# Optimization experiments

Measured on AMD Instinct MI355X. Metric: run time of the kernel, lower is better.

Reference implementation:

```python
import jax, jax.numpy as jnp
import numpy as np

NEG_SLOPE = 0.01  # nn.LeakyReLU default

def _leaky(x):
    return jnp.where(x >= 0, x, NEG_SLOPE * x)

def setup_inputs() -> dict:
    key = jax.random.key(0)
    ks = jax.random.split(key, 8)
    in_ch = 64
    B, H, W = 8, 256, 256
    x = jax.random.normal(ks[0], (B, 2 * in_ch, H, W), dtype=jnp.float32)
    dims = [(64, 128), (32, 64), (16, 32), (8, 16), (4, 8), (2, 4), (1, 2)]
    inp = {"x": x}
    for i, (o, c) in enumerate(dims):
        # kaiming_normal_ fan_out, relu: std = sqrt(2 / fan_out), fan_out = o*1*1
        std = np.sqrt(2.0 / o).astype(np.float32)
        inp[f"w{i+1}"] = jax.random.normal(ks[i + 1], (o, c), dtype=jnp.float32) * std
    return inp

def reference(x, w1, w2, w3, w4, w5, w6, w7):
    # Each 1x1 conv (bias-free) is a per-pixel matmul over channels.
    h = x
    for w in (w1, w2, w3, w4, w5, w6):
        h = _leaky(jnp.einsum('bchw,oc->bohw', h, w))
    out = jnp.einsum('bchw,oc->bohw', h, w7)  # final conv, no activation
    return out
```

## Files before the change

### kernel.cpp

```cpp
#include <hip/hip_runtime.h>


#define NEG_SLOPE 0.01f
constexpr int HW = 65536;

typedef __attribute__((ext_vector_type(8))) short bf16x8;
typedef __attribute__((ext_vector_type(4))) float f32x4;
typedef __attribute__((ext_vector_type(2))) float f32x2;

__device__ __forceinline__ float leaky(float v) { return fmaxf(v, v * NEG_SLOPE); }

__device__ __forceinline__ unsigned pk2(float a, float b) {
    __bf16 ba = (__bf16)a, bb = (__bf16)b;
    unsigned short ua = __builtin_bit_cast(unsigned short, ba);
    unsigned short ub = __builtin_bit_cast(unsigned short, bb);
    return (unsigned)ua | ((unsigned)ub << 16);
}

__device__ __forceinline__ bf16x8 loadA(const float* __restrict__ wsrc, int C, int m, int k) {
    f32x4 lo = *(const f32x4*)(wsrc + m * C + k);
    f32x4 hi = *(const f32x4*)(wsrc + m * C + k + 4);
    union { bf16x8 v; unsigned u[4]; } r;
    r.u[0] = pk2(lo[0], lo[1]); r.u[1] = pk2(lo[2], lo[3]);
    r.u[2] = pk2(hi[0], hi[1]); r.u[3] = pk2(hi[2], hi[3]);
    return r.v;
}

__device__ __forceinline__ void async_cp16(const float* g, float* l) {
    __builtin_amdgcn_global_load_lds((const __attribute__((address_space(1))) unsigned*)g,
                                     (__attribute__((address_space(3))) unsigned*)l,
                                     16, 0, 0);
}

__device__ __forceinline__ void cfence() { asm volatile("" ::: "memory"); }

__global__ __launch_bounds__(256, 2) void fused_wavepipe_kernel(
    const float* __restrict__ x,
    const float* __restrict__ w1, const float* __restrict__ w2,
    const float* __restrict__ w3, const float* __restrict__ w4,
    const float* __restrict__ w5, const float* __restrict__ w6,
    const float* __restrict__ w7, float* __restrict__ out) {
    __shared__ float lds_x[4][4096];
    __shared__ float lds_tw[176];

    const int tid = threadIdx.x;
    if (tid < 128)      lds_tw[tid] = w4[tid];
    else if (tid < 160) lds_tw[tid] = w5[tid - 128];
    else if (tid < 168) lds_tw[tid] = w6[tid - 160];
    else if (tid < 170) lds_tw[tid] = w7[tid - 168];

    const int w    = tid >> 6;
    const int lane = tid & 63;
    const int n    = lane & 15;
    const int q    = lane >> 4;
    const int pl   = lane & 31;

    const int px0   = blockIdx.x * 128;
    const int batch = px0 >> 16;
    const int pin   = px0 & (HW - 1);
    const float* xg = x + (size_t)batch * 128 * HW + pin + w * 32;

    float* Xw = &lds_x[w][0];

    __syncthreads();

    const int r  = lane >> 3;
    const int s4 = (lane & 7) * 4;
    const float* xgr = xg + (size_t)r * HW;

#pragma unroll
    for (int i = 0; i < 4; ++i)
        async_cp16(xgr + (size_t)(i * 8) * HW + (s4 ^ ((i & 3) * 8)), Xw + i * 256);
    cfence();
    __builtin_amdgcn_sched_barrier(0);

    bf16x8 a1[4][4];
#pragma unroll
    for (int Mt = 0; Mt < 4; ++Mt)
#pragma unroll
        for (int kc = 0; kc < 4; ++kc)
            a1[Mt][kc] = loadA(w1, 128, Mt * 16 + n, kc * 32 + q * 8);
    bf16x8 a2[2][2];
#pragma unroll
    for (int Mt = 0; Mt < 2; ++Mt)
#pragma unroll
        for (int kc = 0; kc < 2; ++kc)
            a2[Mt][kc] = loadA(w2, 64, Mt * 16 + n, kc * 32 + q * 8);
    bf16x8 a3 = loadA(w3, 32, n, q * 8);
    cfence();
    __builtin_amdgcn_sched_barrier(0);

#pragma unroll
    for (int i = 4; i < 16; ++i)
        async_cp16(xgr + (size_t)(i * 8) * HW + (s4 ^ ((i & 3) * 8)), Xw + i * 256);
    cfence();
    __builtin_amdgcn_sched_barrier(0);

    f32x4 acc1[4][2];
#pragma unroll
    for (int Mt = 0; Mt < 4; ++Mt)
#pragma unroll
        for (int Nt = 0; Nt < 2; ++Nt) acc1[Mt][Nt] = (f32x4){0.f, 0.f, 0.f, 0.f};

    const int pq = q * 8;
#pragma unroll
    for (int kc = 0; kc < 4; ++kc) {
        if      (kc == 0) asm volatile("s_waitcnt vmcnt(12)" ::: "memory");
        else if (kc == 1) asm volatile("s_waitcnt vmcnt(8)"  ::: "memory");
        else if (kc == 2) asm volatile("s_waitcnt vmcnt(4)"  ::: "memory");
        else              asm volatile("s_waitcnt vmcnt(0)"  ::: "memory");
        __builtin_amdgcn_sched_barrier(0);
        const float* xb = Xw + kc * 1024;
#pragma unroll
        for (int Nt = 0; Nt < 2; ++Nt) {
            const int pxsw = (Nt * 16 + n) ^ pq;
            float t[8];
#pragma unroll
            for (int j = 0; j < 8; ++j)
                t[j] = xb[(pq + j) * 32 + pxsw];
            union { bf16x8 v; unsigned u[4]; } b;
            b.u[0] = pk2(t[0], t[1]); b.u[1] = pk2(t[2], t[3]);
            b.u[2] = pk2(t[4], t[5]); b.u[3] = pk2(t[6], t[7]);
#pragma unroll
            for (int Mt = 0; Mt < 4; ++Mt)
                acc1[Mt][Nt] = __builtin_amdgcn_mfma_f32_16x16x32_bf16(a1[Mt][kc], b.v, acc1[Mt][Nt], 0, 0, 0);
        }
    }
    cfence();

    short* h1 = (short*)Xw;
#pragma unroll
    for (int Mt = 0; Mt < 4; ++Mt)
#pragma unroll
        for (int Nt = 0; Nt < 2; ++Nt) {
            int px = Nt * 16 + n;
            uint2 v;
            v.x = pk2(leaky(acc1[Mt][Nt][0]), leaky(acc1[Mt][Nt][1]));
            v.y = pk2(leaky(acc1[Mt][Nt][2]), leaky(acc1[Mt][Nt][3]));
            *(uint2*)(h1 + px * 68 + Mt * 16 + q * 4) = v;
        }
    cfence();

    f32x4 acc2[2][2];
#pragma unroll
    for (int Mt = 0; Mt < 2; ++Mt)
#pragma unroll
        for (int Nt = 0; Nt < 2; ++Nt) acc2[Mt][Nt] = (f32x4){0.f, 0.f, 0.f, 0.f};
#pragma unroll
    for (int Nt = 0; Nt < 2; ++Nt)
#pragma unroll
        for (int kc = 0; kc < 2; ++kc) {
            int off = (Nt * 16 + n) * 68 + kc * 32 + q * 8;
            uint2 lo = *(const uint2*)(h1 + off);
            uint2 hi = *(const uint2*)(h1 + off + 4);
            union { bf16x8 v; unsigned u[4]; } b;
            b.u[0] = lo.x; b.u[1] = lo.y; b.u[2] = hi.x; b.u[3] = hi.y;
#pragma unroll
            for (int Mt = 0; Mt < 2; ++Mt)
                acc2[Mt][Nt] = __builtin_amdgcn_mfma_f32_16x16x32_bf16(a2[Mt][kc], b.v, acc2[Mt][Nt], 0, 0, 0);
        }
    cfence();

    short* h2 = (short*)Xw;
#pragma unroll
    for (int Mt = 0; Mt < 2; ++Mt)
#pragma unroll
        for (int Nt = 0; Nt < 2; ++Nt) {
            int px = Nt * 16 + n;
            uint2 v;
            v.x = pk2(leaky(acc2[Mt][Nt][0]), leaky(acc2[Mt][Nt][1]));
            v.y = pk2(leaky(acc2[Mt][Nt][2]), leaky(acc2[Mt][Nt][3]));
            *(uint2*)(h2 + px * 36 + Mt * 16 + q * 4) = v;
        }
    cfence();

    f32x4 acc3[2];
#pragma unroll
    for (int Nt = 0; Nt < 2; ++Nt) {
        int off = (Nt * 16 + n) * 36 + q * 8;
        uint2 lo = *(const uint2*)(h2 + off);
        uint2 hi = *(const uint2*)(h2 + off + 4);
        union { bf16x8 v; unsigned u[4]; } b;
        b.u[0] = lo.x; b.u[1] = lo.y; b.u[2] = hi.x; b.u[3] = hi.y;
        f32x4 zero = {0.f, 0.f, 0.f, 0.f};
        acc3[Nt] = __builtin_amdgcn_mfma_f32_16x16x32_bf16(a3, b.v, zero, 0, 0, 0);
    }
    cfence();

    float* h3 = (float*)Xw;
#pragma unroll
    for (int Nt = 0; Nt < 2; ++Nt) {
        int px = Nt * 16 + n;
        f32x2 va = {leaky(acc3[Nt][0]), leaky(acc3[Nt][1])};
        f32x2 vb = {leaky(acc3[Nt][2]), leaky(acc3[Nt][3])};
        *(f32x2*)(h3 + px * 18 + q * 4)     = va;
        *(f32x2*)(h3 + px * 18 + q * 4 + 2) = vb;
    }
    cfence();

    float hh[16];
#pragma unroll
    for (int c = 0; c < 16; ++c) hh[c] = h3[pl * 18 + c];

    float g4[8];
#pragma unroll
    for (int o = 0; o < 8; ++o) {
        float a = 0.f;
#pragma unroll
        for (int c = 0; c < 16; ++c) a = fmaf(lds_tw[o * 16 + c], hh[c], a);
        g4[o] = leaky(a);
    }
    float g5[4];
#pragma unroll
    for (int o = 0; o < 4; ++o) {
        float a = 0.f;
#pragma unroll
        for (int c = 0; c < 8; ++c) a = fmaf(lds_tw[128 + o * 8 + c], g4[c], a);
        g5[o] = leaky(a);
    }
    float g6[2];
#pragma unroll
    for (int o = 0; o < 2; ++o) {
        float a = 0.f;
#pragma unroll
        for (int c = 0; c < 4; ++c) a = fmaf(lds_tw[160 + o * 4 + c], g5[c], a);
        g6[o] = leaky(a);
    }
    float res = fmaf(lds_tw[168], g6[0], lds_tw[169] * g6[1]);
    if (lane < 32) out[px0 + w * 32 + pl] = res;
}

extern "C" void kernel_launch(void* const* d_in, const int* in_sizes, int n_in,
                              void* d_out, int out_size, void* d_ws, size_t ws_size,
                              hipStream_t stream) {
    const float* x  = (const float*)d_in[0];
    const float* w1 = (const float*)d_in[1];
    const float* w2 = (const float*)d_in[2];
    const float* w3 = (const float*)d_in[3];
    const float* w4 = (const float*)d_in[4];
    const float* w5 = (const float*)d_in[5];
    const float* w6 = (const float*)d_in[6];
    const float* w7 = (const float*)d_in[7];
    float* out = (float*)d_out;

    const int P = 8 * 256 * 256;
    fused_wavepipe_kernel<<<P / 128, 256, 0, stream>>>(x, w1, w2, w3, w4, w5, w6, w7, out);
}
```

Measured before the change: 398.9 us.

## Make fused MLP kernel persistent with double-buffered async channel staging

Replaces the one-tile-per-block launch (4096 blocks) with 512 persistent blocks that each process 8 tiles, one per batch. Weight fragments are loaded once per block, and the x loads for the next k-chunk or next tile are issued asynchronously into a two-slot LDS ring while the MFMAs on the current chunk run. The goal is to amortise weight loading and launch overhead and to overlap HBM streaming with compute. In exchange, each wave has fewer loads in flight (at most 8 chunks), the intermediates need a separate LDS scratch area, and the grid may be too small to fill all CUs on a 256-CU part.

```diff
diff --git a/kernel.cpp b/kernel.cpp
--- a/kernel.cpp
+++ b/kernel.cpp
@@ -3,6 +3,9 @@
 
 #define NEG_SLOPE 0.01f
 constexpr int HW = 65536;
+constexpr int GRID = 512;
+constexpr int TPB  = 8;
+constexpr size_t TSTRIDE = (size_t)128 * HW;
 
 typedef __attribute__((ext_vector_type(8))) short bf16x8;
 typedef __attribute__((ext_vector_type(4))) float f32x4;
@@ -34,13 +37,14 @@
 
 __device__ __forceinline__ void cfence() { asm volatile("" ::: "memory"); }
 
-__global__ __launch_bounds__(256, 2) void fused_wavepipe_kernel(
+__global__ __launch_bounds__(256, 2) void fused_persist_kernel(
     const float* __restrict__ x,
     const float* __restrict__ w1, const float* __restrict__ w2,
     const float* __restrict__ w3, const float* __restrict__ w4,
     const float* __restrict__ w5, const float* __restrict__ w6,
     const float* __restrict__ w7, float* __restrict__ out) {
-    __shared__ float lds_x[4][4096];
+    __shared__ float lds_x[4][2][1024];
+    __shared__ float lds_s[4][1088];
     __shared__ float lds_tw[176];
 
     const int tid = threadIdx.x;
@@ -54,25 +58,13 @@
     const int n    = lane & 15;
     const int q    = lane >> 4;
     const int pl   = lane & 31;
-
-    const int px0   = blockIdx.x * 128;
-    const int batch = px0 >> 16;
-    const int pin   = px0 & (HW - 1);
-    const float* xg = x + (size_t)batch * 128 * HW + pin + w * 32;
-
-    float* Xw = &lds_x[w][0];
+    const int r    = lane >> 3;
+    const int s4   = (lane & 7) * 4;
+
+    const int b = blockIdx.x;
+    const float* xg = x + b * 128 + w * 32;
 
     __syncthreads();
-
-    const int r  = lane >> 3;
-    const int s4 = (lane & 7) * 4;
-    const float* xgr = xg + (size_t)r * HW;
-
-#pragma unroll
-    for (int i = 0; i < 4; ++i)
-        async_cp16(xgr + (size_t)(i * 8) * HW + (s4 ^ ((i & 3) * 8)), Xw + i * 256);
-    cfence();
-    __builtin_amdgcn_sched_barrier(0);
 
     bf16x8 a1[4][4];
 #pragma unroll
@@ -90,144 +82,160 @@
     cfence();
     __builtin_amdgcn_sched_barrier(0);
 
-#pragma unroll
-    for (int i = 4; i < 16; ++i)
-        async_cp16(xgr + (size_t)(i * 8) * HW + (s4 ^ ((i & 3) * 8)), Xw + i * 256);
+#define STAGE(BASE, KCX) do {                                                        \
+        const float* gb_ = (BASE) + (size_t)((KCX) * 32 + r) * HW;                   \
+        float* lb_ = &lds_x[w][(KCX) & 1][0];                                        \
+        _Pragma("unroll")                                                            \
+        for (int i_ = 0; i_ < 4; ++i_)                                               \
+            async_cp16(gb_ + (size_t)(i_ * 8) * HW + (s4 ^ (i_ * 8)), lb_ + i_ * 256); \
+    } while (0)
+
+    STAGE(xg, 0);
+    STAGE(xg, 1);
     cfence();
-    __builtin_amdgcn_sched_barrier(0);
-
-    f32x4 acc1[4][2];
-#pragma unroll
-    for (int Mt = 0; Mt < 4; ++Mt)
-#pragma unroll
-        for (int Nt = 0; Nt < 2; ++Nt) acc1[Mt][Nt] = (f32x4){0.f, 0.f, 0.f, 0.f};
 
     const int pq = q * 8;
-#pragma unroll
-    for (int kc = 0; kc < 4; ++kc) {
-        if      (kc == 0) asm volatile("s_waitcnt vmcnt(12)" ::: "memory");
-        else if (kc == 1) asm volatile("s_waitcnt vmcnt(8)"  ::: "memory");
-        else if (kc == 2) asm volatile("s_waitcnt vmcnt(4)"  ::: "memory");
-        else              asm volatile("s_waitcnt vmcnt(0)"  ::: "memory");
-        __builtin_amdgcn_sched_barrier(0);
-        const float* xb = Xw + kc * 1024;
+    for (int it = 0; it < TPB; ++it) {
+        const float* xg_it = xg + (size_t)it * TSTRIDE;
+
+        f32x4 acc1[4][2];
+#pragma unroll
+        for (int Mt = 0; Mt < 4; ++Mt)
+#pragma unroll
+            for (int Nt = 0; Nt < 2; ++Nt) acc1[Mt][Nt] = (f32x4){0.f, 0.f, 0.f, 0.f};
+
+#pragma unroll
+        for (int kc = 0; kc < 4; ++kc) {
+            if (kc == 3 && it == TPB - 1) asm volatile("s_waitcnt vmcnt(0)" ::: "memory");
+            else                          asm volatile("s_waitcnt vmcnt(4)" ::: "memory");
+            __builtin_amdgcn_sched_barrier(0);
+
+            const float* xb = &lds_x[w][kc & 1][0];
+#pragma unroll
+            for (int Nt = 0; Nt < 2; ++Nt) {
+                const int pxsw = (Nt * 16 + n) ^ pq;
+                float t[8];
+#pragma unroll
+                for (int j = 0; j < 8; ++j)
+                    t[j] = xb[(pq + j) * 32 + pxsw];
+                union { bf16x8 v; unsigned u[4]; } bb;
+                bb.u[0] = pk2(t[0], t[1]); bb.u[1] = pk2(t[2], t[3]);
+                bb.u[2] = pk2(t[4], t[5]); bb.u[3] = pk2(t[6], t[7]);
+#pragma unroll
+                for (int Mt = 0; Mt < 4; ++Mt)
+                    acc1[Mt][Nt] = __builtin_amdgcn_mfma_f32_16x16x32_bf16(a1[Mt][kc], bb.v, acc1[Mt][Nt], 0, 0, 0);
+            }
+            __builtin_amdgcn_sched_barrier(0);
+
+            if (kc < 2)            STAGE(xg_it, kc + 2);
+            else if (it < TPB - 1) STAGE(xg_it + TSTRIDE, kc - 2);
+            cfence();
+        }
+
+        float* Sw = &lds_s[w][0];
+        short* h1 = (short*)Sw;
+#pragma unroll
+        for (int Mt = 0; Mt < 4; ++Mt)
+#pragma unroll
+            for (int Nt = 0; Nt < 2; ++Nt) {
+                int px = Nt * 16 + n;
+                uint2 v;
+                v.x = pk2(leaky(acc1[Mt][Nt][0]), leaky(acc1[Mt][Nt][1]));
+                v.y = pk2(leaky(acc1[Mt][Nt][2]), leaky(acc1[Mt][Nt][3]));
+                *(uint2*)(h1 + px * 68 + Mt * 16 + q * 4) = v;
+            }
+        cfence();
+
+        f32x4 acc2[2][2];
+#pragma unroll
+        for (int Mt = 0; Mt < 2; ++Mt)
+#pragma unroll
+            for (int Nt = 0; Nt < 2; ++Nt) acc2[Mt][Nt] = (f32x4){0.f, 0.f, 0.f, 0.f};
+#pragma unroll
+        for (int Nt = 0; Nt < 2; ++Nt)
+#pragma unroll
+            for (int kc = 0; kc < 2; ++kc) {
+                int off = (Nt * 16 + n) * 68 + kc * 32 + q * 8;
+                uint2 lo = *(const uint2*)(h1 + off);
+                uint2 hi = *(const uint2*)(h1 + off + 4);
+                union { bf16x8 v; unsigned u[4]; } bb;
+                bb.u[0] = lo.x; bb.u[1] = lo.y; bb.u[2] = hi.x; bb.u[3] = hi.y;
+#pragma unroll
+                for (int Mt = 0; Mt < 2; ++Mt)
+                    acc2[Mt][Nt] = __builtin_amdgcn_mfma_f32_16x16x32_bf16(a2[Mt][kc], bb.v, acc2[Mt][Nt], 0, 0, 0);
+            }
+        cfence();
+
+        short* h2 = (short*)Sw;
+#pragma unroll
+        for (int Mt = 0; Mt < 2; ++Mt)
+#pragma unroll
+            for (int Nt = 0; Nt < 2; ++Nt) {
+                int px = Nt * 16 + n;
+                uint2 v;
+                v.x = pk2(leaky(acc2[Mt][Nt][0]), leaky(acc2[Mt][Nt][1]));
+                v.y = pk2(leaky(acc2[Mt][Nt][2]), leaky(acc2[Mt][Nt][3]));
+                *(uint2*)(h2 + px * 36 + Mt * 16 + q * 4) = v;
+            }
+        cfence();
+
+        f32x4 acc3[2];
 #pragma unroll
         for (int Nt = 0; Nt < 2; ++Nt) {
-            const int pxsw = (Nt * 16 + n) ^ pq;
-            float t[8];
-#pragma unroll
-            for (int j = 0; j < 8; ++j)
-                t[j] = xb[(pq + j) * 32 + pxsw];
-            union { bf16x8 v; unsigned u[4]; } b;
-            b.u[0] = pk2(t[0], t[1]); b.u[1] = pk2(t[2], t[3]);
-            b.u[2] = pk2(t[4], t[5]); b.u[3] = pk2(t[6], t[7]);
-#pragma unroll
-            for (int Mt = 0; Mt < 4; ++Mt)
-                acc1[Mt][Nt] = __builtin_amdgcn_mfma_f32_16x16x32_bf16(a1[Mt][kc], b.v, acc1[Mt][Nt], 0, 0, 0);
-        }
-    }
-    cfence();
-
-    short* h1 = (short*)Xw;
-#pragma unroll
-    for (int Mt = 0; Mt < 4; ++Mt)
+            int off = (Nt * 16 + n) * 36 + q * 8;
+            uint2 lo = *(const uint2*)(h2 + off);
+            uint2 hi = *(const uint2*)(h2 + off + 4);
+            union { bf16x8 v; unsigned u[4]; } bb;
+            bb.u[0] = lo.x; bb.u[1] = lo.y; bb.u[2] = hi.x; bb.u[3] = hi.y;
+            f32x4 zero = {0.f, 0.f, 0.f, 0.f};
+            acc3[Nt] = __builtin_amdgcn_mfma_f32_16x16x32_bf16(a3, bb.v, zero, 0, 0, 0);
+        }
+        cfence();
+
+        float* h3 = Sw;
 #pragma unroll
         for (int Nt = 0; Nt < 2; ++Nt) {
             int px = Nt * 16 + n;
-            uint2 v;
-            v.x = pk2(leaky(acc1[Mt][Nt][0]), leaky(acc1[Mt][Nt][1]));
-            v.y = pk2(leaky(acc1[Mt][Nt][2]), leaky(acc1[Mt][Nt][3]));
-            *(uint2*)(h1 + px * 68 + Mt * 16 + q * 4) = v;
-        }
-    cfence();
-
-    f32x4 acc2[2][2];
-#pragma unroll
-    for (int Mt = 0; Mt < 2; ++Mt)
-#pragma unroll
-        for (int Nt = 0; Nt < 2; ++Nt) acc2[Mt][Nt] = (f32x4){0.f, 0.f, 0.f, 0.f};
-#pragma unroll
-    for (int Nt = 0; Nt < 2; ++Nt)
-#pragma unroll
-        for (int kc = 0; kc < 2; ++kc) {
-            int off = (Nt * 16 + n) * 68 + kc * 32 + q * 8;
-            uint2 lo = *(const uint2*)(h1 + off);
-            uint2 hi = *(const uint2*)(h1 + off + 4);
-            union { bf16x8 v; unsigned u[4]; } b;
-            b.u[0] = lo.x; b.u[1] = lo.y; b.u[2] = hi.x; b.u[3] = hi.y;
-#pragma unroll
-            for (int Mt = 0; Mt < 2; ++Mt)
-                acc2[Mt][Nt] = __builtin_amdgcn_mfma_f32_16x16x32_bf16(a2[Mt][kc], b.v, acc2[Mt][Nt], 0, 0, 0);
-        }
-    cfence();
-
-    short* h2 = (short*)Xw;
-#pragma unroll
-    for (int Mt = 0; Mt < 2; ++Mt)
-#pragma unroll
-        for (int Nt = 0; Nt < 2; ++Nt) {
-            int px = Nt * 16 + n;
-            uint2 v;
-            v.x = pk2(leaky(acc2[Mt][Nt][0]), leaky(acc2[Mt][Nt][1]));
-            v.y = pk2(leaky(acc2[Mt][Nt][2]), leaky(acc2[Mt][Nt][3]));
-            *(uint2*)(h2 + px * 36 + Mt * 16 + q * 4) = v;
-        }
-    cfence();
-
-    f32x4 acc3[2];
-#pragma unroll
-    for (int Nt = 0; Nt < 2; ++Nt) {
-        int off = (Nt * 16 + n) * 36 + q * 8;
-        uint2 lo = *(const uint2*)(h2 + off);
-        uint2 hi = *(const uint2*)(h2 + off + 4);
-        union { bf16x8 v; unsigned u[4]; } b;
-        b.u[0] = lo.x; b.u[1] = lo.y; b.u[2] = hi.x; b.u[3] = hi.y;
-        f32x4 zero = {0.f, 0.f, 0.f, 0.f};
-        acc3[Nt] = __builtin_amdgcn_mfma_f32_16x16x32_bf16(a3, b.v, zero, 0, 0, 0);
+            f32x2 va = {leaky(acc3[Nt][0]), leaky(acc3[Nt][1])};
+            f32x2 vb = {leaky(acc3[Nt][2]), leaky(acc3[Nt][3])};
+            *(f32x2*)(h3 + px * 18 + q * 4)     = va;
+            *(f32x2*)(h3 + px * 18 + q * 4 + 2) = vb;
+        }
+        cfence();
+
+        float hh[16];
+#pragma unroll
+        for (int c = 0; c < 16; ++c) hh[c] = h3[pl * 18 + c];
+
+        float g4[8];
+#pragma unroll
+        for (int o = 0; o < 8; ++o) {
+            float a = 0.f;
+#pragma unroll
+            for (int c = 0; c < 16; ++c) a = fmaf(lds_tw[o * 16 + c], hh[c], a);
+            g4[o] = leaky(a);
+        }
+        float g5[4];
+#pragma unroll
+        for (int o = 0; o < 4; ++o) {
+            float a = 0.f;
+#pragma unroll
+            for (int c = 0; c < 8; ++c) a = fmaf(lds_tw[128 + o * 8 + c], g4[c], a);
+            g5[o] = leaky(a);
+        }
+        float g6[2];
+#pragma unroll
+        for (int o = 0; o < 2; ++o) {
+            float a = 0.f;
+#pragma unroll
+            for (int c = 0; c < 4; ++c) a = fmaf(lds_tw[160 + o * 4 + c], g5[c], a);
+            g6[o] = leaky(a);
+        }
+        float res = fmaf(lds_tw[168], g6[0], lds_tw[169] * g6[1]);
+        if (lane < 32) out[b * 128 + it * 65536 + w * 32 + pl] = res;
+        cfence();
     }
-    cfence();
-
-    float* h3 = (float*)Xw;
-#pragma unroll
-    for (int Nt = 0; Nt < 2; ++Nt) {
-        int px = Nt * 16 + n;
-        f32x2 va = {leaky(acc3[Nt][0]), leaky(acc3[Nt][1])};
-        f32x2 vb = {leaky(acc3[Nt][2]), leaky(acc3[Nt][3])};
-        *(f32x2*)(h3 + px * 18 + q * 4)     = va;
-        *(f32x2*)(h3 + px * 18 + q * 4 + 2) = vb;
-    }
-    cfence();
-
-    float hh[16];
-#pragma unroll
-    for (int c = 0; c < 16; ++c) hh[c] = h3[pl * 18 + c];
-
-    float g4[8];
-#pragma unroll
-    for (int o = 0; o < 8; ++o) {
-        float a = 0.f;
-#pragma unroll
-        for (int c = 0; c < 16; ++c) a = fmaf(lds_tw[o * 16 + c], hh[c], a);
-        g4[o] = leaky(a);
-    }
-    float g5[4];
-#pragma unroll
-    for (int o = 0; o < 4; ++o) {
-        float a = 0.f;
-#pragma unroll
-        for (int c = 0; c < 8; ++c) a = fmaf(lds_tw[128 + o * 8 + c], g4[c], a);
-        g5[o] = leaky(a);
-    }
-    float g6[2];
-#pragma unroll
-    for (int o = 0; o < 2; ++o) {
-        float a = 0.f;
-#pragma unroll
-        for (int c = 0; c < 4; ++c) a = fmaf(lds_tw[160 + o * 4 + c], g5[c], a);
-        g6[o] = leaky(a);
-    }
-    float res = fmaf(lds_tw[168], g6[0], lds_tw[169] * g6[1]);
-    if (lane < 32) out[px0 + w * 32 + pl] = res;
+#undef STAGE
 }
 
 extern "C" void kernel_launch(void* const* d_in, const int* in_sizes, int n_in,
@@ -243,6 +251,5 @@
     const float* w7 = (const float*)d_in[7];
     float* out = (float*)d_out;
 
-    const int P = 8 * 256 * 256;
-    fused_wavepipe_kernel<<<P / 128, 256, 0, stream>>>(x, w1, w2, w3, w4, w5, w6, w7, out);
-}
+    fused_persist_kernel<<<GRID, 256, 0, stream>>>(x, w1, w2, w3, w4, w5, w6, w7, out);
+}
```

New measurement: 380.2 us. 4.7% less time.
